# Kernel optimization log

Measured on AMD Instinct MI355X. Metric: run time of the kernel, lower is better.

The kernel has to match this reference:

```python
import jax, jax.numpy as jnp
import numpy as np

N_EXPERTS = 8
TOPK = 2
D_MODEL = 1024
D_FF = 4096

def setup_inputs() -> dict:
    key = jax.random.key(0)
    k_x, k_g, k_1, k_2 = jax.random.split(key, 4)
    x = jax.random.normal(k_x, (4, 2048, D_MODEL), dtype=jnp.float32)
    Wg = jax.random.normal(k_g, (D_MODEL, N_EXPERTS), dtype=jnp.float32) * 0.02
    W1 = jax.random.normal(k_1, (N_EXPERTS, D_MODEL, D_FF), dtype=jnp.float32) * 0.02
    W2 = jax.random.normal(k_2, (N_EXPERTS, D_FF, D_MODEL), dtype=jnp.float32) * 0.02
    return {"x": x, "Wg": Wg, "W1": W1, "W2": W2}

def reference(x, Wg, W1, W2):
    B, S, D = x.shape
    xt = x.reshape(-1, D)                      # [T, D]
    T = xt.shape[0]
    logits = xt @ Wg                            # [T, E]
    vals, idx = jax.lax.top_k(logits, TOPK)     # [T, K]
    w = jax.nn.softmax(vals, axis=-1)           # renormalize over selected experts
    # scatter top-k weights into dense [T, E] gate matrix (zeros elsewhere)
    gates = jnp.zeros((T, N_EXPERTS), dtype=x.dtype).at[jnp.arange(T)[:, None], idx].set(w)
    out = jnp.zeros_like(xt)
    for e in range(N_EXPERTS):                  # fixed small loop over experts
        h = jax.nn.silu(xt @ W1[e]) @ W2[e]     # [T, D]
        out = out + gates[:, e:e+1] * h
    return out.reshape(B, S, D)
```

## Files before the change

kernel.cpp:

```cpp
#include <hip/hip_runtime.h>
#include <hip/hip_bf16.h>
#include <math.h>

#define T_TOK 8192
#define DM 1024
#define DF 4096
#define NE 8
#define MAXT 72

typedef __attribute__((ext_vector_type(4))) float  f32x4;
typedef __attribute__((ext_vector_type(8))) short  s16x8;
typedef __attribute__((ext_vector_type(8))) unsigned short u16x8;

__device__ __forceinline__ unsigned short f2bf(float f) {
    unsigned int u = __builtin_bit_cast(unsigned int, f);
    u = (u + 0x7FFFu + ((u >> 16) & 1u)) >> 16;
    return (unsigned short)u;
}

#define GLDS16(gptr, lptr)                                                         \
    __builtin_amdgcn_global_load_lds(                                              \
        (const __attribute__((address_space(1))) void*)(gptr),                     \
        (__attribute__((address_space(3))) void*)(lptr), 16, 0, 0)

#define BAR() asm volatile("s_barrier" ::: "memory")

template<int W>
__device__ __forceinline__ void waitvm() {
    if constexpr (W == 8)      asm volatile("s_waitcnt vmcnt(8)" ::: "memory");
    else                       asm volatile("s_waitcnt vmcnt(0)" ::: "memory");
}

__global__ __launch_bounds__(256) void route_kernel(
    const float* __restrict__ x, const float* __restrict__ Wg,
    int* __restrict__ counts, int* __restrict__ lists, float* __restrict__ pw)
{
    int tok  = (int)((blockIdx.x * blockDim.x + threadIdx.x) >> 6);
    int lane = threadIdx.x & 63;
    if (tok >= T_TOK) return;

    const float* xr = x + (size_t)tok * DM;
    float acc[NE];
#pragma unroll
    for (int e = 0; e < NE; ++e) acc[e] = 0.f;

    for (int i = lane; i < DM; i += 64) {
        float xv = xr[i];
        const float* wr = Wg + (size_t)i * NE;
#pragma unroll
        for (int e = 0; e < NE; ++e) acc[e] += xv * wr[e];
    }
#pragma unroll
    for (int e = 0; e < NE; ++e) {
#pragma unroll
        for (int off = 32; off > 0; off >>= 1)
            acc[e] += __shfl_xor(acc[e], off, 64);
    }

    if (lane == 0) {
        int i0 = 0; float v0 = acc[0];
#pragma unroll
        for (int e = 1; e < NE; ++e) if (acc[e] > v0) { v0 = acc[e]; i0 = e; }
        int i1 = -1; float v1 = -INFINITY;
#pragma unroll
        for (int e = 0; e < NE; ++e) if (e != i0 && acc[e] > v1) { v1 = acc[e]; i1 = e; }
        float e1 = __expf(v1 - v0);
        float s  = 1.f + e1;
        int p0 = tok * 2, p1 = tok * 2 + 1;
        pw[p0] = 1.f / s;
        pw[p1] = e1 / s;
        int pos0 = atomicAdd(&counts[i0], 1);
        lists[i0 * T_TOK + pos0] = p0;
        int pos1 = atomicAdd(&counts[i1], 1);
        lists[i1 * T_TOK + pos1] = p1;
    }
}

__global__ void offsets_kernel(const int* __restrict__ counts, int* __restrict__ offsets,
                               unsigned* __restrict__ table, int* __restrict__ ntp)
{
    if (threadIdx.x == 0) {
        int s = 0, ti = 0;
        for (int e = 0; e < NE; ++e) {
            offsets[e] = s;
            int cnt = counts[e];
            for (int t0 = 0; t0 < cnt; t0 += 256)
                table[ti++] = ((unsigned)e << 20) | (unsigned)t0;
            s += cnt;
        }
        ntp[0] = ti;
        for (; ti < MAXT; ++ti) table[ti] = 0xFFFFFFFFu;
    }
}

__global__ __launch_bounds__(256) void conv_x_kernel(
    const float* __restrict__ x, unsigned short* __restrict__ xb)
{
    size_t i = ((size_t)blockIdx.x * 256 + threadIdx.x) * 8;
    float4 v0 = *reinterpret_cast<const float4*>(x + i);
    float4 v1 = *reinterpret_cast<const float4*>(x + i + 4);
    u16x8 o;
    o[0] = f2bf(v0.x); o[1] = f2bf(v0.y); o[2] = f2bf(v0.z); o[3] = f2bf(v0.w);
    o[4] = f2bf(v1.x); o[5] = f2bf(v1.y); o[6] = f2bf(v1.z); o[7] = f2bf(v1.w);
    *reinterpret_cast<u16x8*>(xb + i) = o;
}

template<int K, int N>
__global__ __launch_bounds__(256) void transpose_conv_kernel(
    const float* __restrict__ W, unsigned short* __restrict__ Wt)
{
    int e  = blockIdx.z;
    int k0 = blockIdx.x * 64;
    int n0 = blockIdx.y * 64;
    const float* We = W + (size_t)e * K * N;
    unsigned short* Wte = Wt + (size_t)e * K * N;

    __shared__ unsigned short t[64][73];
    int c4 = (threadIdx.x & 15) * 4;
    int r  = threadIdx.x >> 4;
#pragma unroll
    for (int i = 0; i < 4; ++i) {
        int rr = r + i * 16;
        float4 v = *reinterpret_cast<const float4*>(We + (size_t)(k0 + rr) * N + n0 + c4);
        t[rr][c4 + 0] = f2bf(v.x); t[rr][c4 + 1] = f2bf(v.y);
        t[rr][c4 + 2] = f2bf(v.z); t[rr][c4 + 3] = f2bf(v.w);
    }
    __syncthreads();
    int kc = (threadIdx.x & 7) * 8;
    int rn = threadIdx.x >> 3;
#pragma unroll
    for (int i = 0; i < 2; ++i) {
        int nn = rn + i * 32;
        u16x8 o;
#pragma unroll
        for (int j = 0; j < 8; ++j) o[j] = t[kc + j][nn];
        *reinterpret_cast<u16x8*>(Wte + (size_t)(n0 + nn) * K + k0 + kc) = o;
    }
}

template<int N, int K, int SPLITK, bool IS_G1>
__global__ __launch_bounds__(512, 2) void moe_gemm8(
    const unsigned short* __restrict__ A,
    const unsigned short* __restrict__ Wt,
    const int* __restrict__ counts, const int* __restrict__ offsets,
    const int* __restrict__ lists, const unsigned* __restrict__ table,
    const int* __restrict__ ntp, const float* __restrict__ pw,
    unsigned short* __restrict__ Hout, float* __restrict__ Oout)
{
    constexpr int NT  = N / 256;
    constexpr int PAN = NT * SPLITK;
    constexpr int KS  = K / SPLITK;
    constexpr int NKT = KS / 64;
    static_assert(NKT >= 2, "pipeline depth");

    __shared__ __attribute__((aligned(16))) char lds[131072];

    int ntl  = ntp[0];
    int live = ntl * PAN;
    int orig = blockIdx.x;
    if (orig >= live) return;
    int q = live >> 3, r = live & 7;
    int xq = orig & 7, ib = orig >> 3;
    int work = (xq < r ? xq * (q + 1) : r * (q + 1) + (xq - r) * q) + ib;
    int rt    = work / PAN;
    int panel = work - rt * PAN;
    int nt    = (SPLITK == 2) ? (panel >> 1) : panel;
    int sk    = (SPLITK == 2) ? (panel & 1) : 0;
    int koff  = sk * KS;

    unsigned te = table[rt];
    int e     = (int)(te >> 20);
    int slot0 = (int)(te & 0xFFFFFu);
    int cnt   = counts[e];
    int off   = offsets[e];
    int ntile = nt * 256;

    int tid  = threadIdx.x;
    int lane = tid & 63;
    int wid  = tid >> 6;
    int wm = wid >> 2;
    int wn = wid & 3;
    int l15 = lane & 15, l4 = lane >> 4;

    const unsigned short* Be = Wt + (size_t)e * N * K;

    int ssw = ((tid & 7) ^ ((tid >> 3) & 7)) * 8;
    int r0  = tid >> 3;
    unsigned aOff0, aOff1, aOff2, aOff3;
    {
#pragma unroll
        for (int u = 0; u < 4; ++u) {
            int sl = slot0 + u * 64 + r0;
            unsigned grow;
            if (IS_G1) grow = (sl < cnt) ? (unsigned)(lists[e * T_TOK + sl] >> 1) : 0u;
            else       grow = (unsigned)(off + ((sl < cnt) ? sl : slot0));
            unsigned v = grow * (unsigned)K + (unsigned)(koff + ssw);
            if (u == 0) aOff0 = v; else if (u == 1) aOff1 = v;
            else if (u == 2) aOff2 = v; else aOff3 = v;
        }
    }
    unsigned bOff0 = (unsigned)(ntile + 0   + r0) * (unsigned)K + (unsigned)(koff + ssw);
    unsigned bOff1 = (unsigned)(ntile + 64  + r0) * (unsigned)K + (unsigned)(koff + ssw);
    unsigned bOff2 = (unsigned)(ntile + 128 + r0) * (unsigned)K + (unsigned)(koff + ssw);
    unsigned bOff3 = (unsigned)(ntile + 192 + r0) * (unsigned)K + (unsigned)(koff + ssw);

    auto stage = [&](int s, int kt) {
        int ko = kt * 64;
        char* dA = lds + s * 32768 + tid * 16;
        char* dB = lds + 65536 + s * 32768 + tid * 16;
        GLDS16(A + aOff0 + ko, dA);
        GLDS16(A + aOff1 + ko, dA + 8192);
        GLDS16(A + aOff2 + ko, dA + 16384);
        GLDS16(A + aOff3 + ko, dA + 24576);
        GLDS16(Be + bOff0 + ko, dB);
        GLDS16(Be + bOff1 + ko, dB + 8192);
        GLDS16(Be + bOff2 + ko, dB + 16384);
        GLDS16(Be + bOff3 + ko, dB + 24576);
    };

    int swz  = (l4 ^ (l15 & 7)) * 16;
    int aRdB = (wm * 128 + l15) * 128 + swz;
    int bRdB = (wn * 64  + l15) * 128 + swz;

    f32x4 acc[8][4];
#pragma unroll
    for (int m = 0; m < 8; ++m)
#pragma unroll
        for (int n = 0; n < 4; ++n) acc[m][n] = (f32x4){0.f, 0.f, 0.f, 0.f};

    auto tilestep = [&](int s) {
        const char* Ab = lds + s * 32768;
        const char* Bb = lds + 65536 + s * 32768;
#pragma unroll
        for (int kh = 0; kh < 2; ++kh) {
            const int khx = kh * 64;
            s16x8 bf[4];
#pragma unroll
            for (int n = 0; n < 4; ++n)
                bf[n] = *reinterpret_cast<const s16x8*>(Bb + ((bRdB + n * 2048) ^ khx));
#pragma unroll
            for (int mh = 0; mh < 2; ++mh) {
                s16x8 af[4];
#pragma unroll
                for (int m = 0; m < 4; ++m)
                    af[m] = *reinterpret_cast<const s16x8*>(Ab + ((aRdB + (mh * 4 + m) * 2048) ^ khx));
                __builtin_amdgcn_s_setprio(1);
#pragma unroll
                for (int n = 0; n < 4; ++n)
#pragma unroll
                    for (int m = 0; m < 4; ++m)
                        acc[mh * 4 + m][n] = __builtin_amdgcn_mfma_f32_16x16x32_bf16(
                            af[m], bf[n], acc[mh * 4 + m][n], 0, 0, 0);
                __builtin_amdgcn_s_setprio(0);
                BAR();
            }
        }
    };

    stage(0, 0);
    stage(1, 1);
    waitvm<8>();
    BAR();
    for (int kt = 0; kt < NKT; ++kt) {
        tilestep(kt & 1);
        if (kt + 2 < NKT) {
            stage(kt & 1, kt + 2);
            waitvm<8>();
        } else {
            waitvm<0>();
        }
        BAR();
    }

#pragma unroll
    for (int m = 0; m < 8; ++m) {
        int trow = wm * 128 + m * 16 + l4 * 4;
#pragma unroll
        for (int rr = 0; rr < 4; ++rr) {
            int slot = slot0 + trow + rr;
            if (slot >= cnt) continue;
            if (IS_G1) {
                unsigned short* hr = Hout + (size_t)(off + slot) * N;
#pragma unroll
                for (int n = 0; n < 4; ++n) {
                    int col = ntile + wn * 64 + n * 16 + l15;
                    float v = acc[m][n][rr];
                    float s = v / (1.f + __expf(-v));
                    hr[col] = f2bf(s);
                }
            } else {
                int p = lists[e * T_TOK + slot];
                float w = pw[p];
                float* orow = Oout + (size_t)(p >> 1) * DM;
#pragma unroll
                for (int n = 0; n < 4; ++n) {
                    int col = ntile + wn * 64 + n * 16 + l15;
                    atomicAdd(orow + col, w * acc[m][n][rr]);
                }
            }
        }
    }
}

#define BMF 16
#define BFF 256
__global__ __launch_bounds__(256) void expert_gemm_f32(
    const float* __restrict__ x, const float* __restrict__ W1, const float* __restrict__ W2,
    const int* __restrict__ counts, const int* __restrict__ lists, const float* __restrict__ pw,
    float* __restrict__ out)
{
    int e    = blockIdx.y;
    int tile = blockIdx.x;
    int cnt  = counts[e];
    int start = tile * BMF;
    if (start >= cnt) return;

    __shared__ float xs[BMF][DM];
    __shared__ float hs[BMF][BFF];
    __shared__ int   toks[BMF];
    __shared__ float wgt[BMF];

    int tid = threadIdx.x;
    int nm  = cnt - start; if (nm > BMF) nm = BMF;

    if (tid < BMF) {
        if (tid < nm) {
            int p = lists[e * T_TOK + start + tid];
            toks[tid] = p >> 1;
            wgt[tid]  = pw[p];
        } else { toks[tid] = -1; wgt[tid] = 0.f; }
    }
    __syncthreads();
    for (int m = 0; m < BMF; ++m) {
        int t = toks[m];
        const float* xr = (t >= 0) ? (x + (size_t)t * DM) : nullptr;
        for (int i = tid; i < DM; i += 256) xs[m][i] = (t >= 0) ? xr[i] : 0.f;
    }
    __syncthreads();

    const float* W1e = W1 + (size_t)e * DM * DF;
    const float* W2e = W2 + (size_t)e * DF * DM;
    float acc[BMF][4];
#pragma unroll
    for (int m = 0; m < BMF; ++m)
#pragma unroll
        for (int c = 0; c < 4; ++c) acc[m][c] = 0.f;

    for (int fc = 0; fc < DF; fc += BFF) {
        float hacc[BMF];
#pragma unroll
        for (int m = 0; m < BMF; ++m) hacc[m] = 0.f;
        const float* w1col = W1e + fc + tid;
#pragma unroll 4
        for (int i = 0; i < DM; ++i) {
            float w1v = w1col[(size_t)i * DF];
#pragma unroll
            for (int m = 0; m < BMF; ++m) hacc[m] += xs[m][i] * w1v;
        }
        __syncthreads();
#pragma unroll
        for (int m = 0; m < BMF; ++m) {
            float v = hacc[m];
            hs[m][tid] = v / (1.f + __expf(-v));
        }
        __syncthreads();
        const float* w2base = W2e + (size_t)fc * DM + tid * 4;
        for (int f = 0; f < BFF; ++f) {
            float4 w2v = *reinterpret_cast<const float4*>(w2base + (size_t)f * DM);
#pragma unroll
            for (int m = 0; m < BMF; ++m) {
                float h = hs[m][f];
                acc[m][0] += h * w2v.x; acc[m][1] += h * w2v.y;
                acc[m][2] += h * w2v.z; acc[m][3] += h * w2v.w;
            }
        }
        __syncthreads();
    }
    int c0 = tid * 4;
#pragma unroll
    for (int m = 0; m < BMF; ++m) {
        int t = toks[m];
        if (t < 0) continue;
        float w = wgt[m];
        float* op = out + (size_t)t * DM + c0;
        atomicAdd(op + 0, w * acc[m][0]);
        atomicAdd(op + 1, w * acc[m][1]);
        atomicAdd(op + 2, w * acc[m][2]);
        atomicAdd(op + 3, w * acc[m][3]);
    }
}

extern "C" void kernel_launch(void* const* d_in, const int* in_sizes, int n_in,
                              void* d_out, int out_size, void* d_ws, size_t ws_size,
                              hipStream_t stream)
{
    const float* x  = (const float*)d_in[0];
    const float* Wg = (const float*)d_in[1];
    const float* W1 = (const float*)d_in[2];
    const float* W2 = (const float*)d_in[3];
    float* out = (float*)d_out;

    char* ws = (char*)d_ws;
    int*      counts  = (int*)(ws + 0);
    int*      offsets = (int*)(ws + 64);
    int*      ntp     = (int*)(ws + 128);
    unsigned* table   = (unsigned*)(ws + 256);
    int*      lists   = (int*)(ws + 2048);
    float*    pw      = (float*)(ws + 2048 + 262144);

    const size_t o_xb  = 524288;
    const size_t sz_xb = (size_t)T_TOK * DM * 2;
    const size_t o_w1t = o_xb + sz_xb;
    const size_t sz_w  = (size_t)NE * DM * DF * 2;
    const size_t o_w2t = o_w1t + sz_w;
    const size_t o_h   = o_w2t + sz_w;
    const size_t sz_h  = (size_t)(2 * T_TOK) * DF * 2;
    const size_t NEEDED = o_h + sz_h;

    hipMemsetAsync(counts, 0, 64, stream);
    route_kernel<<<T_TOK / 4, 256, 0, stream>>>(x, Wg, counts, lists, pw);

    if (ws_size >= NEEDED) {
        unsigned short* xb  = (unsigned short*)(ws + o_xb);
        unsigned short* w1t = (unsigned short*)(ws + o_w1t);
        unsigned short* w2t = (unsigned short*)(ws + o_w2t);
        unsigned short* H   = (unsigned short*)(ws + o_h);

        hipMemsetAsync(d_out, 0, (size_t)out_size * sizeof(float), stream);
        offsets_kernel<<<1, 64, 0, stream>>>(counts, offsets, table, ntp);
        conv_x_kernel<<<(T_TOK * DM) / (256 * 8), 256, 0, stream>>>(x, xb);
        {
            dim3 g(DM / 64, DF / 64, NE);
            transpose_conv_kernel<DM, DF><<<g, 256, 0, stream>>>(W1, w1t);
        }
        {
            dim3 g(DF / 64, DM / 64, NE);
            transpose_conv_kernel<DF, DM><<<g, 256, 0, stream>>>(W2, w2t);
        }
        moe_gemm8<DF, DM, 1, true><<<dim3(MAXT * (DF / 256)), 512, 0, stream>>>(
            xb, w1t, counts, offsets, lists, table, ntp, pw, H, nullptr);
        moe_gemm8<DM, DF, 2, false><<<dim3(MAXT * (DM / 256) * 2), 512, 0, stream>>>(
            H, w2t, counts, offsets, lists, table, ntp, pw, nullptr, out);
    } else {
        hipMemsetAsync(d_out, 0, (size_t)out_size * sizeof(float), stream);
        dim3 grid(T_TOK / BMF, NE);
        expert_gemm_f32<<<grid, 256, 0, stream>>>(x, W1, W2, counts, lists, pw, out);
    }
}
```

Baseline: 810.2 us.

## Restructure MoE GEMM into 4-stage half-tile pipeline with interleaved A/B prefetch

The MoE GEMM main loop now stages half k-tiles of 32 elements in a 4-slot LDS ring instead of full 64-wide tiles double-buffered. A and B global-to-LDS loads are issued separately and interleaved between the MFMA groups, with a three-deep prefetch and finer vmcnt waits. The goal is to hide global-load latency better and spread memory traffic across the compute. The XOR swizzle on LDS reads is dropped, which may bring back bank conflicts, and the loop now issues more barriers per tile.

```diff
diff --git a/kernel.cpp b/kernel.cpp
--- a/kernel.cpp
+++ b/kernel.cpp
@@ -28,6 +28,7 @@
 template<int W>
 __device__ __forceinline__ void waitvm() {
     if constexpr (W == 8)      asm volatile("s_waitcnt vmcnt(8)" ::: "memory");
+    else if constexpr (W == 4) asm volatile("s_waitcnt vmcnt(4)" ::: "memory");
     else                       asm volatile("s_waitcnt vmcnt(0)" ::: "memory");
 }
 
@@ -139,7 +140,7 @@
 }
 
 template<int N, int K, int SPLITK, bool IS_G1>
-__global__ __launch_bounds__(512, 2) void moe_gemm8(
+__global__ __launch_bounds__(512, 2) void moe_gemm9(
     const unsigned short* __restrict__ A,
     const unsigned short* __restrict__ Wt,
     const int* __restrict__ counts, const int* __restrict__ offsets,
@@ -151,7 +152,8 @@
     constexpr int PAN = NT * SPLITK;
     constexpr int KS  = K / SPLITK;
     constexpr int NKT = KS / 64;
-    static_assert(NKT >= 2, "pipeline depth");
+    constexpr int NHS = 2 * NKT;
+    static_assert(NKT >= 3, "pipeline depth");
 
     __shared__ __attribute__((aligned(16))) char lds[131072];
 
@@ -184,43 +186,40 @@
 
     const unsigned short* Be = Wt + (size_t)e * N * K;
 
-    int ssw = ((tid & 7) ^ ((tid >> 3) & 7)) * 8;
-    int r0  = tid >> 3;
-    unsigned aOff0, aOff1, aOff2, aOff3;
+    int kg8 = (tid & 3) * 8;
+    int r0  = tid >> 2;
+    unsigned aOff0, aOff1;
     {
 #pragma unroll
-        for (int u = 0; u < 4; ++u) {
-            int sl = slot0 + u * 64 + r0;
+        for (int u = 0; u < 2; ++u) {
+            int sl = slot0 + u * 128 + r0;
             unsigned grow;
             if (IS_G1) grow = (sl < cnt) ? (unsigned)(lists[e * T_TOK + sl] >> 1) : 0u;
             else       grow = (unsigned)(off + ((sl < cnt) ? sl : slot0));
-            unsigned v = grow * (unsigned)K + (unsigned)(koff + ssw);
-            if (u == 0) aOff0 = v; else if (u == 1) aOff1 = v;
-            else if (u == 2) aOff2 = v; else aOff3 = v;
-        }
-    }
-    unsigned bOff0 = (unsigned)(ntile + 0   + r0) * (unsigned)K + (unsigned)(koff + ssw);
-    unsigned bOff1 = (unsigned)(ntile + 64  + r0) * (unsigned)K + (unsigned)(koff + ssw);
-    unsigned bOff2 = (unsigned)(ntile + 128 + r0) * (unsigned)K + (unsigned)(koff + ssw);
-    unsigned bOff3 = (unsigned)(ntile + 192 + r0) * (unsigned)K + (unsigned)(koff + ssw);
-
-    auto stage = [&](int s, int kt) {
-        int ko = kt * 64;
-        char* dA = lds + s * 32768 + tid * 16;
-        char* dB = lds + 65536 + s * 32768 + tid * 16;
-        GLDS16(A + aOff0 + ko, dA);
-        GLDS16(A + aOff1 + ko, dA + 8192);
-        GLDS16(A + aOff2 + ko, dA + 16384);
-        GLDS16(A + aOff3 + ko, dA + 24576);
-        GLDS16(Be + bOff0 + ko, dB);
-        GLDS16(Be + bOff1 + ko, dB + 8192);
-        GLDS16(Be + bOff2 + ko, dB + 16384);
-        GLDS16(Be + bOff3 + ko, dB + 24576);
+            unsigned v = grow * (unsigned)K + (unsigned)(koff + kg8);
+            if (u == 0) aOff0 = v; else aOff1 = v;
+        }
+    }
+    unsigned bOff0 = (unsigned)(ntile + r0)       * (unsigned)K + (unsigned)(koff + kg8);
+    unsigned bOff1 = (unsigned)(ntile + 128 + r0) * (unsigned)K + (unsigned)(koff + kg8);
+
+    auto SA = [&](int hs) {
+        if (hs < NHS) {
+            char* d = lds + (hs & 3) * 16384 + tid * 16;
+            GLDS16(A + aOff0 + hs * 32, d);
+            GLDS16(A + aOff1 + hs * 32, d + 8192);
+        }
     };
-
-    int swz  = (l4 ^ (l15 & 7)) * 16;
-    int aRdB = (wm * 128 + l15) * 128 + swz;
-    int bRdB = (wn * 64  + l15) * 128 + swz;
+    auto SB = [&](int hs) {
+        if (hs < NHS) {
+            char* d = lds + 65536 + (hs & 3) * 16384 + tid * 16;
+            GLDS16(Be + bOff0 + hs * 32, d);
+            GLDS16(Be + bOff1 + hs * 32, d + 8192);
+        }
+    };
+
+    int aRd = (wm * 128 + l15) * 64 + l4 * 16;
+    int bRd = (wn * 64  + l15) * 64 + l4 * 16;
 
     f32x4 acc[8][4];
 #pragma unroll
@@ -228,47 +227,54 @@
 #pragma unroll
         for (int n = 0; n < 4; ++n) acc[m][n] = (f32x4){0.f, 0.f, 0.f, 0.f};
 
-    auto tilestep = [&](int s) {
-        const char* Ab = lds + s * 32768;
-        const char* Bb = lds + 65536 + s * 32768;
-#pragma unroll
-        for (int kh = 0; kh < 2; ++kh) {
-            const int khx = kh * 64;
-            s16x8 bf[4];
-#pragma unroll
-            for (int n = 0; n < 4; ++n)
-                bf[n] = *reinterpret_cast<const s16x8*>(Bb + ((bRdB + n * 2048) ^ khx));
-#pragma unroll
-            for (int mh = 0; mh < 2; ++mh) {
-                s16x8 af[4];
-#pragma unroll
-                for (int m = 0; m < 4; ++m)
-                    af[m] = *reinterpret_cast<const s16x8*>(Ab + ((aRdB + (mh * 4 + m) * 2048) ^ khx));
-                __builtin_amdgcn_s_setprio(1);
-#pragma unroll
-                for (int n = 0; n < 4; ++n)
-#pragma unroll
-                    for (int m = 0; m < 4; ++m)
-                        acc[mh * 4 + m][n] = __builtin_amdgcn_mfma_f32_16x16x32_bf16(
-                            af[m], bf[n], acc[mh * 4 + m][n], 0, 0, 0);
-                __builtin_amdgcn_s_setprio(0);
-                BAR();
-            }
-        }
+    s16x8 af[4], bf[4];
+    auto loadA = [&](int hs, int mh) {
+        const char* Ab = lds + (hs & 3) * 16384;
+#pragma unroll
+        for (int m = 0; m < 4; ++m)
+            af[m] = *reinterpret_cast<const s16x8*>(Ab + aRd + mh * 4096 + m * 1024);
     };
-
-    stage(0, 0);
-    stage(1, 1);
+    auto loadB = [&](int hs) {
+        const char* Bb = lds + 65536 + (hs & 3) * 16384;
+#pragma unroll
+        for (int n = 0; n < 4; ++n)
+            bf[n] = *reinterpret_cast<const s16x8*>(Bb + bRd + n * 1024);
+    };
+    auto mfma16 = [&](int mh) {
+        __builtin_amdgcn_s_setprio(1);
+#pragma unroll
+        for (int n = 0; n < 4; ++n)
+#pragma unroll
+            for (int m = 0; m < 4; ++m)
+                acc[mh * 4 + m][n] = __builtin_amdgcn_mfma_f32_16x16x32_bf16(
+                    af[m], bf[n], acc[mh * 4 + m][n], 0, 0, 0);
+        __builtin_amdgcn_s_setprio(0);
+    };
+
+    SA(0); SB(0); SA(1); SB(1); SA(2); SB(2);
     waitvm<8>();
     BAR();
+
     for (int kt = 0; kt < NKT; ++kt) {
-        tilestep(kt & 1);
-        if (kt + 2 < NKT) {
-            stage(kt & 1, kt + 2);
-            waitvm<8>();
-        } else {
-            waitvm<0>();
-        }
+        int hs0 = 2 * kt, hs1 = 2 * kt + 1;
+        loadB(hs0); loadA(hs0, 0); SA(2 * kt + 3);
+        BAR();
+        mfma16(0);
+        BAR();
+        loadA(hs0, 1); SB(2 * kt + 3);
+        BAR();
+        mfma16(1);
+        if (kt < NKT - 1) waitvm<8>(); else waitvm<0>();
+        BAR();
+        loadB(hs1); loadA(hs1, 0); SA(2 * kt + 4);
+        BAR();
+        mfma16(0);
+        BAR();
+        loadA(hs1, 1); SB(2 * kt + 4);
+        BAR();
+        mfma16(1);
+        if (kt < NKT - 2)       waitvm<8>();
+        else if (kt == NKT - 2) waitvm<4>();
         BAR();
     }
 
@@ -437,9 +443,9 @@
             dim3 g(DF / 64, DM / 64, NE);
             transpose_conv_kernel<DF, DM><<<g, 256, 0, stream>>>(W2, w2t);
         }
-        moe_gemm8<DF, DM, 1, true><<<dim3(MAXT * (DF / 256)), 512, 0, stream>>>(
+        moe_gemm9<DF, DM, 1, true><<<dim3(MAXT * (DF / 256)), 512, 0, stream>>>(
             xb, w1t, counts, offsets, lists, table, ntp, pw, H, nullptr);
-        moe_gemm8<DM, DF, 2, false><<<dim3(MAXT * (DM / 256) * 2), 512, 0, stream>>>(
+        moe_gemm9<DM, DF, 2, false><<<dim3(MAXT * (DM / 256) * 2), 512, 0, stream>>>(
             H, w2t, counts, offsets, lists, table, ntp, pw, nullptr, out);
     } else {
         hipMemsetAsync(d_out, 0, (size_t)out_size * sizeof(float), stream);
```

After: 782.2 us. 3.5% less time.
